# Kernel optimization log

Measured on AMD Instinct MI355X. Metric: run time of the kernel, lower is better.

## Reference

```python
import jax, jax.numpy as jnp
import numpy as np

B, LQ, LKV, LT, C, H = 4, 1024, 1344, 320, 768, 12
DH = C // H
SCALE = DH ** -0.5
HID = 4 * C
EPS = 1e-5


def _ln(x, g, b):
    m = jnp.mean(x, axis=-1, keepdims=True)
    v = jnp.mean((x - m) ** 2, axis=-1, keepdims=True)
    return (x - m) * jax.lax.rsqrt(v + EPS) * g + b


def setup_inputs() -> dict:
    key = jax.random.key(0)
    ks = jax.random.split(key, 16)
    s = lambda k, shape, sc=0.02: jax.random.normal(k, shape, dtype=jnp.float32) * sc
    return {
        "tem_mask": s(ks[0], (B, LT, C), 1.0),
        "q": s(ks[1], (B, LQ, C), 1.0),
        "kv": s(ks[2], (B, LKV, C), 1.0),
        "attn_pos": s(ks[3], (1, H, LQ, LKV), 1.0),
        "ln1q_g": jnp.ones((C,)), "ln1q_b": jnp.zeros((C,)),
        "ln1kv_g": jnp.ones((C,)), "ln1kv_b": jnp.zeros((C,)),
        "Wq": s(ks[4], (C, C)), "bq": jnp.zeros((C,)),
        "Wkv": s(ks[5], (C, 2 * C)), "bkv": jnp.zeros((2 * C,)),
        "Wp": s(ks[6], (C, C)), "bp": jnp.zeros((C,)),
        "ln2_g": jnp.ones((C,)), "ln2_b": jnp.zeros((C,)),
        "W1": s(ks[7], (C, HID)), "b1": jnp.zeros((HID,)),
        "W2": s(ks[8], (HID, C)), "b2": jnp.zeros((C,)),
    }


def reference(tem_mask, q, kv, attn_pos, ln1q_g, ln1q_b, ln1kv_g, ln1kv_b,
              Wq, bq, Wkv, bkv, Wp, bp, ln2_g, ln2_b, W1, b1, W2, b2):
    qn = _ln(q, ln1q_g, ln1q_b)
    kvn = _ln(kv, ln1kv_g, ln1kv_b)
    # projections (attn_pos_encoding_only branch)
    qh = (qn @ Wq + bq).reshape(B, LQ, H, DH).transpose(0, 2, 1, 3)  # (B,H,Lq,Dh)
    kvp = kvn @ Wkv + bkv
    k, v = kvp[:, :, :C], kvp[:, :, C:]
    v = v.at[:, :LT, :].add(tem_mask)  # add template mask to template tokens
    kh = k.reshape(B, LKV, H, DH).transpose(0, 2, 1, 3)
    vh = v.reshape(B, LKV, H, DH).transpose(0, 2, 1, 3)
    attn = jnp.einsum('bhqd,bhkd->bhqk', qh, kh) * SCALE + attn_pos
    attn = jax.nn.softmax(attn, axis=-1)
    x = jnp.einsum('bhqk,bhkd->bhqd', attn, vh)
    x = x.transpose(0, 2, 1, 3).reshape(B, LQ, C)
    x = x @ Wp + bp
    q = q + x  # residual 1 (drop_path = Identity, dropout eval)
    h = _ln(q, ln2_g, ln2_b)
    h = jax.nn.gelu(h @ W1 + b1, approximate=False)
    h = h @ W2 + b2
    return q + h
```

## Files before the change

### kernel.cpp

```cpp
#include <hip/hip_runtime.h>
#include <hip/hip_bf16.h>
#include <math.h>

typedef __bf16 bf16x8 __attribute__((ext_vector_type(8)));
typedef float f32x4 __attribute__((ext_vector_type(4)));

__device__ __forceinline__ __hip_bfloat16 f2bf(float v){ return __float2bfloat16(v); }

__device__ __forceinline__ void gload16(const void* g, void* l){
  __builtin_amdgcn_global_load_lds(
      (const __attribute__((address_space(1))) void*)g,
      (__attribute__((address_space(3))) void*)l, 16, 0, 0);
}

__global__ void transpose_f2b(const float* __restrict__ in,
                              __hip_bfloat16* __restrict__ out, int K, int N){
  __shared__ float tile[32][33];
  int tx = threadIdx.x, ty = threadIdx.y;
  int n0 = blockIdx.x*32, k0 = blockIdx.y*32;
#pragma unroll
  for(int i=0;i<4;i++) tile[ty+i*8][tx] = in[(size_t)(k0+ty+i*8)*N + n0+tx];
  __syncthreads();
#pragma unroll
  for(int i=0;i<4;i++) out[(size_t)(n0+ty+i*8)*K + k0+tx] = f2bf(tile[tx][ty+i*8]);
}

__global__ __launch_bounds__(256) void transpose_vt(const __hip_bfloat16* __restrict__ vbuf,
                                                    __hip_bfloat16* __restrict__ vt){
  __shared__ __hip_bfloat16 tl[64][72];
  const int bh = blockIdx.x;
  const int kt = blockIdx.y;
  const int b = bh / 12, h = bh % 12;
  const int tid = threadIdx.x;
  const int r = tid >> 3, c = (tid & 7) * 8;
#pragma unroll
  for(int j=0;j<2;j++){
    uint4 v = *(const uint4*)(vbuf + ((size_t)(b*1344 + kt*64 + r + j*32))*768 + h*64 + c);
    *(uint4*)&tl[r + j*32][c] = v;
  }
  __syncthreads();
#pragma unroll
  for(int j=0;j<2;j++){
    int d = r + j*32;
    __hip_bfloat16 tmp[8];
#pragma unroll
    for(int i=0;i<8;i++) tmp[i] = tl[c + i][d];
    *(uint4*)(vt + ((size_t)(bh*64 + d))*1344 + kt*64 + c) = *(const uint4*)tmp;
  }
}

__global__ __launch_bounds__(256) void ln_kernel(const float* __restrict__ in,
    const float* __restrict__ g, const float* __restrict__ b,
    __hip_bfloat16* __restrict__ out){
  int row = blockIdx.x, t = threadIdx.x;
  const float* rp = in + (size_t)row*768;
  float x0 = rp[t], x1 = rp[t+256], x2 = rp[t+512];
  float s = x0+x1+x2, ss = x0*x0+x1*x1+x2*x2;
#pragma unroll
  for(int o=32;o>0;o>>=1){ s += __shfl_down(s,o); ss += __shfl_down(ss,o); }
  __shared__ float red[10];
  if((t&63)==0){ red[t>>6]=s; red[4+(t>>6)]=ss; }
  __syncthreads();
  if(t==0){
    float S=red[0]+red[1]+red[2]+red[3], SS=red[4]+red[5]+red[6]+red[7];
    float m=S*(1.f/768.f);
    red[8]=m; red[9]=SS*(1.f/768.f)-m*m;
  }
  __syncthreads();
  float m=red[8], r=rsqrtf(red[9]+1e-5f);
  __hip_bfloat16* op = out + (size_t)row*768;
  op[t]     = f2bf((x0-m)*r*g[t]     + b[t]);
  op[t+256] = f2bf((x1-m)*r*g[t+256] + b[t+256]);
  op[t+512] = f2bf((x2-m)*r*g[t+512] + b[t+512]);
}

template<int BM, int EPI>
__global__ __launch_bounds__(256) void gemm_gl(
    const __hip_bfloat16* __restrict__ A, const __hip_bfloat16* __restrict__ BT,
    const float* __restrict__ bias, int M, int N, int K,
    void* __restrict__ out, const void* __restrict__ aux0, void* __restrict__ out2){
  constexpr int NF = (BM==128)?4:2;
  __shared__ char sA[2][BM*128];
  __shared__ char sB[2][128*128];
  const int tid = threadIdx.x;
  const int l = tid & 63, w = tid >> 6;
  const int lg = l >> 4, li = l & 15;
  const int wrow = (BM==128)? (w>>1)*64 : 0;
  const int wcol = (BM==128)? (w&1)*64 : w*32;
  const int bm = blockIdx.x * BM;
  const int bn = blockIdx.y * 128;
  const int arow = w*(BM/4) + (l>>3);
  const int brow = w*32 + (l>>3);
  const int scol = ((((l&7)*16) ^ ((l>>3)<<4)) >> 1);

  auto stage = [&](int buf, int kt){
    const int k0 = kt*64;
#pragma unroll
    for(int i=0;i<BM/32;i++)
      gload16(A  + (size_t)(bm+arow+i*8)*K + k0 + scol, sA[buf] + (w*(BM/4))*128 + i*1024);
#pragma unroll
    for(int i=0;i<4;i++)
      gload16(BT + (size_t)(bn+brow+i*8)*K + k0 + scol, sB[buf] + (w*32)*128 + i*1024);
  };

  f32x4 acc[4][NF] = {};
  const int nk = K >> 6;
  stage(0, 0);
  __syncthreads();
  for(int kt=0; kt<nk; ++kt){
    const int cur = kt & 1;
    if(kt+1 < nk) stage(cur^1, kt+1);
#pragma unroll
    for(int kk=0;kk<2;kk++){
      const int kb = kk*64 + lg*16;
      bf16x8 af[4], bfr[NF];
#pragma unroll
      for(int m=0;m<4;m++){
        int row = wrow+m*16+li;
        af[m] = *(const bf16x8*)(sA[cur] + row*128 + (kb ^ ((row&7)<<4)));
      }
#pragma unroll
      for(int n=0;n<NF;n++){
        int row = wcol+n*16+li;
        bfr[n] = *(const bf16x8*)(sB[cur] + row*128 + (kb ^ ((row&7)<<4)));
      }
#pragma unroll
      for(int m=0;m<4;m++)
#pragma unroll
        for(int n=0;n<NF;n++)
          acc[m][n] = __builtin_amdgcn_mfma_f32_16x16x32_bf16(af[m], bfr[n], acc[m][n],0,0,0);
    }
    __syncthreads();
  }
#pragma unroll
  for(int m=0;m<4;m++){
#pragma unroll
    for(int n=0;n<NF;n++){
#pragma unroll
      for(int r=0;r<4;r++){
        int row = bm + wrow + m*16 + lg*4 + r;
        int col = bn + wcol + n*16 + li;
        float v = acc[m][n][r] + bias[col];
        if constexpr(EPI==0){
          ((__hip_bfloat16*)out)[(size_t)row*N + col] = f2bf(v * 0.125f);
        } else if constexpr(EPI==1){
          if(col < 768){
            ((__hip_bfloat16*)out)[(size_t)row*768 + col] = f2bf(v);
          } else {
            int c = col - 768;
            int bb = row / 1344, ii = row % 1344;
            if(ii < 320) v += ((const float*)aux0)[((size_t)bb*320 + ii)*768 + c];
            ((__hip_bfloat16*)out2)[(size_t)row*768 + c] = f2bf(v);
          }
        } else if constexpr(EPI==2){
          v += ((const float*)aux0)[(size_t)row*N + col];
          ((float*)out)[(size_t)row*N + col] = v;
        } else if constexpr(EPI==3){
          float gl = 0.5f * v * (1.0f + erff(v * 0.70710678118654752f));
          ((__hip_bfloat16*)out)[(size_t)row*N + col] = f2bf(gl);
        } else {
          v += ((const float*)aux0)[(size_t)row*N + col];
          ((float*)out)[(size_t)row*N + col] = v;
        }
      }
    }
  }
}

__global__ __launch_bounds__(256) void attn_kernel(
    const __hip_bfloat16* __restrict__ qh,
    const __hip_bfloat16* __restrict__ kb,
    const __hip_bfloat16* __restrict__ vt,
    const float* __restrict__ pos,
    __hip_bfloat16* __restrict__ xo){
  __shared__ char sK[2][8192];
  __shared__ char sV[2][8192];
  __shared__ char sP[4][2048];
  const int bid = blockIdx.x;
  const int qt = bid & 15, h = (bid >> 4) % 12, b = bid / 192;
  const int q0 = qt * 64;
  const int tid = threadIdx.x;
  const int l = tid & 63, w = tid >> 6;
  const int lg = l >> 4, li = l & 15;

  const int srow = w*16 + (l>>3);
  const int soff = (((l&7)*16) ^ ((l>>3)<<4)) >> 1;
  const __hip_bfloat16* ksrc = kb + ((size_t)b*1344 + srow)*768 + h*64 + soff;
  const __hip_bfloat16* vsrc = vt + ((size_t)(b*12+h)*64 + srow)*1344 + soff;

  bf16x8 aq[2];
  {
    const char* qp = (const char*)(qh + ((size_t)(b*1024 + q0 + w*16 + li))*768 + h*64);
    aq[0] = *(const bf16x8*)(qp + lg*16);
    aq[1] = *(const bf16x8*)(qp + 64 + lg*16);
  }
  const size_t posbase = ((size_t)h*1024 + q0 + w*16 + lg*4)*1344 + li;

  f32x4 accO[4] = {};
  float mrun[4], lrun[4];
#pragma unroll
  for(int r=0;r<4;r++){ mrun[r] = -1e30f; lrun[r] = 0.f; }

  auto stage = [&](int buf, int t){
    const size_t ko = (size_t)t*64*768;
    const size_t vo = (size_t)t*64;
    gload16(ksrc + ko,          sK[buf] + w*2048);
    gload16(ksrc + ko + 8*768,  sK[buf] + w*2048 + 1024);
    gload16(vsrc + vo,          sV[buf] + w*2048);
    gload16(vsrc + vo + 8*1344, sV[buf] + w*2048 + 1024);
  };
  auto ldpos = [&](int t, float pr[4][4]){
    const float* pp = pos + posbase + (size_t)t*64;
#pragma unroll
    for(int n=0;n<4;n++)
#pragma unroll
      for(int r=0;r<4;r++)
        pr[n][r] = __builtin_nontemporal_load(pp + (size_t)r*1344 + n*16);
  };

  float posr[4][4];
  ldpos(0, posr);
  stage(0, 0);
  __syncthreads();

  char* sPw = sP[w];
  for(int t=0; t<21; ++t){
    const int cur = t & 1;
    f32x4 accS[4] = {};
#pragma unroll
    for(int kk=0; kk<2; ++kk){
      const int kbyte = kk*64 + lg*16;
#pragma unroll
      for(int n=0;n<4;n++){
        int row = n*16 + li;
        bf16x8 bkf = *(const bf16x8*)(sK[cur] + row*128 + (kbyte ^ ((row&7)<<4)));
        accS[n] = __builtin_amdgcn_mfma_f32_16x16x32_bf16(aq[kk], bkf, accS[n], 0,0,0);
      }
    }
    if(t < 20) stage(cur^1, t+1);
    float npos[4][4];
    if(t < 20) ldpos(t+1, npos);

    float p[4][4], mt[4];
#pragma unroll
    for(int r=0;r<4;r++) mt[r] = -1e30f;
#pragma unroll
    for(int n=0;n<4;n++)
#pragma unroll
      for(int r=0;r<4;r++){
        float s = accS[n][r] + posr[n][r];
        p[n][r] = s;
        mt[r] = fmaxf(mt[r], s);
      }
#pragma unroll
    for(int r=0;r<4;r++){
#pragma unroll
      for(int o=1;o<16;o<<=1) mt[r] = fmaxf(mt[r], __shfl_xor(mt[r], o));
      float mnew = fmaxf(mrun[r], mt[r]);
      float sf = __expf(mrun[r]-mnew);
      mrun[r] = mnew;
      lrun[r] *= sf;
#pragma unroll
      for(int n=0;n<4;n++) accO[n][r] *= sf;
      float rs = 0.f;
#pragma unroll
      for(int n=0;n<4;n++){ p[n][r] = __expf(p[n][r]-mnew); rs += p[n][r]; }
#pragma unroll
      for(int o=1;o<16;o<<=1) rs += __shfl_xor(rs, o);
      lrun[r] += rs;
    }
#pragma unroll
    for(int n=0;n<4;n++)
#pragma unroll
      for(int r=0;r<4;r++){
        int qi = lg*4 + r, kj = n*16 + li;
        *(__hip_bfloat16*)(sPw + qi*128 + ((kj*2) ^ ((qi&7)<<4))) = f2bf(p[n][r]);
      }
#pragma unroll
    for(int kk=0; kk<2; ++kk){
      const int kbyte = kk*64 + lg*16;
      bf16x8 pa = *(const bf16x8*)(sPw + li*128 + (kbyte ^ ((li&7)<<4)));
#pragma unroll
      for(int n=0;n<4;n++){
        int d = n*16 + li;
        bf16x8 bvf = *(const bf16x8*)(sV[cur] + d*128 + (kbyte ^ ((d&7)<<4)));
        accO[n] = __builtin_amdgcn_mfma_f32_16x16x32_bf16(pa, bvf, accO[n], 0,0,0);
      }
    }
    if(t < 20){
#pragma unroll
      for(int n=0;n<4;n++)
#pragma unroll
        for(int r=0;r<4;r++) posr[n][r] = npos[n][r];
    }
    __syncthreads();
  }
#pragma unroll
  for(int n=0;n<4;n++)
#pragma unroll
    for(int r=0;r<4;r++){
      int row = b*1024 + q0 + w*16 + lg*4 + r;
      int col = h*64 + n*16 + li;
      xo[(size_t)row*768 + col] = f2bf(accO[n][r] / lrun[r]);
    }
}

extern "C" void kernel_launch(void* const* d_in, const int* in_sizes, int n_in,
                              void* d_out, int out_size, void* d_ws, size_t ws_size,
                              hipStream_t stream){
  const float* tem   = (const float*)d_in[0];
  const float* qin   = (const float*)d_in[1];
  const float* kvin  = (const float*)d_in[2];
  const float* pos   = (const float*)d_in[3];
  const float* ln1qg = (const float*)d_in[4];
  const float* ln1qb = (const float*)d_in[5];
  const float* ln1kg = (const float*)d_in[6];
  const float* ln1kb = (const float*)d_in[7];
  const float* Wq    = (const float*)d_in[8];
  const float* bq    = (const float*)d_in[9];
  const float* Wkv   = (const float*)d_in[10];
  const float* bkv   = (const float*)d_in[11];
  const float* Wp    = (const float*)d_in[12];
  const float* bp    = (const float*)d_in[13];
  const float* ln2g  = (const float*)d_in[14];
  const float* ln2b  = (const float*)d_in[15];
  const float* W1    = (const float*)d_in[16];
  const float* b1    = (const float*)d_in[17];
  const float* W2    = (const float*)d_in[18];
  const float* b2    = (const float*)d_in[19];

  char* ws = (char*)d_ws; size_t off = 0;
  auto alloc = [&](size_t n){ char* p = ws + off; off = (off + n + 255) & ~(size_t)255; return p; };
  __hip_bfloat16* WqT  = (__hip_bfloat16*)alloc((size_t)768*768*2);
  __hip_bfloat16* WkvT = (__hip_bfloat16*)alloc((size_t)1536*768*2);
  __hip_bfloat16* WpT  = (__hip_bfloat16*)alloc((size_t)768*768*2);
  __hip_bfloat16* W1T  = (__hip_bfloat16*)alloc((size_t)3072*768*2);
  __hip_bfloat16* W2T  = (__hip_bfloat16*)alloc((size_t)768*3072*2);
  __hip_bfloat16* qn   = (__hip_bfloat16*)alloc((size_t)4096*768*2);
  char* poolBase = alloc((size_t)5376*768*2*3 + (size_t)4096*768*2);
  __hip_bfloat16* kvn  = (__hip_bfloat16*)poolBase;
  __hip_bfloat16* kbuf = kvn  + (size_t)5376*768;
  __hip_bfloat16* vbuf = kbuf + (size_t)5376*768;
  __hip_bfloat16* qhb  = vbuf + (size_t)5376*768;
  __hip_bfloat16* xat  = (__hip_bfloat16*)alloc((size_t)4096*768*2);
  float*          x1f  = (float*)alloc((size_t)4096*768*4);
  __hip_bfloat16* vt   = kvn;
  __hip_bfloat16* hln  = qn;
  __hip_bfloat16* h1   = kvn;

  dim3 tb(32,8);
  transpose_f2b<<<dim3(768/32, 768/32),  tb, 0, stream>>>(Wq,  WqT,  768, 768);
  transpose_f2b<<<dim3(1536/32, 768/32), tb, 0, stream>>>(Wkv, WkvT, 768, 1536);
  transpose_f2b<<<dim3(768/32, 768/32),  tb, 0, stream>>>(Wp,  WpT,  768, 768);
  transpose_f2b<<<dim3(3072/32, 768/32), tb, 0, stream>>>(W1,  W1T,  768, 3072);
  transpose_f2b<<<dim3(768/32, 3072/32), tb, 0, stream>>>(W2,  W2T,  3072, 768);

  ln_kernel<<<4096, 256, 0, stream>>>(qin,  ln1qg, ln1qb, qn);
  ln_kernel<<<5376, 256, 0, stream>>>(kvin, ln1kg, ln1kb, kvn);

  gemm_gl<64,0> <<<dim3(64, 6),  256, 0, stream>>>(qn,  WqT,  bq,  4096, 768,  768,  qhb, nullptr, nullptr);
  gemm_gl<128,1><<<dim3(42, 12), 256, 0, stream>>>(kvn, WkvT, bkv, 5376, 1536, 768,  kbuf, tem, vbuf);
  transpose_vt<<<dim3(48, 21), 256, 0, stream>>>(vbuf, vt);

  attn_kernel<<<768, 256, 0, stream>>>(qhb, kbuf, vt, pos, xat);

  gemm_gl<64,2> <<<dim3(64, 6),  256, 0, stream>>>(xat, WpT,  bp,  4096, 768,  768,  x1f, qin, nullptr);
  ln_kernel<<<4096, 256, 0, stream>>>(x1f, ln2g, ln2b, hln);
  gemm_gl<128,3><<<dim3(32, 24), 256, 0, stream>>>(hln, W1T,  b1,  4096, 3072, 768,  h1, nullptr, nullptr);
  gemm_gl<64,4> <<<dim3(64, 6),  256, 0, stream>>>(h1,  W2T,  b2,  4096, 768,  3072, (float*)d_out, x1f, nullptr);
}
```

Before: 258.3 us.

## Restructure attention blocks to share attn_pos tile across batches with 32-key steps

The attention kernel now uses 512-thread blocks covering one head and a 32-row query tile for all four batch elements. Each wave pair handles one batch, and the grid mapping is arranged so that blocks sharing the same attn_pos rows are adjacent. The key tile shrinks from 64 to 32, giving 42 iterations unrolled in pairs with ping-pong position registers. The loop issues prefetches before compute and replaces __syncthreads with an explicit vmcnt wait plus a raw barrier. The aim is better pos reuse through cache and finer-grained overlap, at the cost of more iterations and barriers, a tricky manual waitcnt, and half the block count.

```diff
diff --git a/kernel.cpp b/kernel.cpp
--- a/kernel.cpp
+++ b/kernel.cpp
@@ -167,34 +167,38 @@
   }
 }
 
-__global__ __launch_bounds__(256) void attn_kernel(
+__global__ __launch_bounds__(512) void attn_kernel(
     const __hip_bfloat16* __restrict__ qh,
     const __hip_bfloat16* __restrict__ kb,
     const __hip_bfloat16* __restrict__ vt,
     const float* __restrict__ pos,
     __hip_bfloat16* __restrict__ xo){
-  __shared__ char sK[2][8192];
-  __shared__ char sV[2][8192];
-  __shared__ char sP[4][2048];
+  __shared__ char sK[2][4][4096];
+  __shared__ char sV[2][4][4096];
+  __shared__ char sP[8][1024];
   const int bid = blockIdx.x;
-  const int qt = bid & 15, h = (bid >> 4) % 12, b = bid / 192;
-  const int q0 = qt * 64;
+  const int u = (bid & 7)*3 + ((bid >> 3) >> 4);
+  const int v = (bid >> 3) & 15;
+  const int h = u >> 1;
+  const int q0 = ((u & 1)*16 + v) * 32;
   const int tid = threadIdx.x;
   const int l = tid & 63, w = tid >> 6;
+  const int bt = w >> 1, qhv = w & 1;
   const int lg = l >> 4, li = l & 15;
 
-  const int srow = w*16 + (l>>3);
-  const int soff = (((l&7)*16) ^ ((l>>3)<<4)) >> 1;
-  const __hip_bfloat16* ksrc = kb + ((size_t)b*1344 + srow)*768 + h*64 + soff;
-  const __hip_bfloat16* vsrc = vt + ((size_t)(b*12+h)*64 + srow)*1344 + soff;
+  const int kelem = ((((l&7)*16) ^ ((l>>3)<<4)) >> 1);
+  const int velem = ((((l&3)*16) ^ (((l>>2)&3)<<4)) >> 1);
+  const __hip_bfloat16* ksrc = kb + ((size_t)bt*1344 + qhv*16 + (l>>3))*768 + h*64 + kelem;
+  const __hip_bfloat16* vsrc = vt + (((size_t)(bt*12+h))*64 + qhv*32 + (l>>2))*1344 + velem;
+  char* sKb = nullptr; char* sVb = nullptr;
 
   bf16x8 aq[2];
   {
-    const char* qp = (const char*)(qh + ((size_t)(b*1024 + q0 + w*16 + li))*768 + h*64);
+    const char* qp = (const char*)(qh + ((size_t)(bt*1024 + q0 + qhv*16 + li))*768 + h*64);
     aq[0] = *(const bf16x8*)(qp + lg*16);
     aq[1] = *(const bf16x8*)(qp + 64 + lg*16);
   }
-  const size_t posbase = ((size_t)h*1024 + q0 + w*16 + lg*4)*1344 + li;
+  const size_t posbase = ((size_t)h*1024 + q0 + qhv*16 + lg*4)*1344 + li;
 
   f32x4 accO[4] = {};
   float mrun[4], lrun[4];
@@ -202,50 +206,52 @@
   for(int r=0;r<4;r++){ mrun[r] = -1e30f; lrun[r] = 0.f; }
 
   auto stage = [&](int buf, int t){
-    const size_t ko = (size_t)t*64*768;
-    const size_t vo = (size_t)t*64;
-    gload16(ksrc + ko,          sK[buf] + w*2048);
-    gload16(ksrc + ko + 8*768,  sK[buf] + w*2048 + 1024);
-    gload16(vsrc + vo,          sV[buf] + w*2048);
-    gload16(vsrc + vo + 8*1344, sV[buf] + w*2048 + 1024);
+    const size_t ko = (size_t)t*32*768;
+    const size_t vo = (size_t)t*32;
+#pragma unroll
+    for(int i=0;i<2;i++)
+      gload16(ksrc + ko + (size_t)i*8*768, sK[buf][bt] + qhv*2048 + i*1024);
+#pragma unroll
+    for(int i=0;i<2;i++)
+      gload16(vsrc + vo + (size_t)i*16*1344, sV[buf][bt] + qhv*2048 + i*1024);
   };
-  auto ldpos = [&](int t, float pr[4][4]){
-    const float* pp = pos + posbase + (size_t)t*64;
-#pragma unroll
-    for(int n=0;n<4;n++)
+  auto ldpos = [&](int t, float pr[2][4]){
+    const float* pp = pos + posbase + (size_t)t*32;
+#pragma unroll
+    for(int n=0;n<2;n++)
 #pragma unroll
       for(int r=0;r<4;r++)
         pr[n][r] = __builtin_nontemporal_load(pp + (size_t)r*1344 + n*16);
   };
 
-  float posr[4][4];
-  ldpos(0, posr);
+  char* sPw = sP[w];
+  float pA[2][4], pB[2][4];
+  ldpos(0, pA);
   stage(0, 0);
   __syncthreads();
 
-  char* sPw = sP[w];
-  for(int t=0; t<21; ++t){
-    const int cur = t & 1;
-    f32x4 accS[4] = {};
+  auto body = [&](int t, int cur, float posr[2][4], float npos[2][4]){
+    const bool more = (t < 41);
+    if(more) stage(cur^1, t+1);
+    asm volatile("" ::: "memory");
+    if(more) ldpos(t+1, npos);
+
+    f32x4 accS[2] = {};
 #pragma unroll
     for(int kk=0; kk<2; ++kk){
       const int kbyte = kk*64 + lg*16;
 #pragma unroll
-      for(int n=0;n<4;n++){
+      for(int n=0;n<2;n++){
         int row = n*16 + li;
-        bf16x8 bkf = *(const bf16x8*)(sK[cur] + row*128 + (kbyte ^ ((row&7)<<4)));
+        bf16x8 bkf = *(const bf16x8*)(sK[cur][bt] + row*128 + (kbyte ^ ((row&7)<<4)));
         accS[n] = __builtin_amdgcn_mfma_f32_16x16x32_bf16(aq[kk], bkf, accS[n], 0,0,0);
       }
     }
-    if(t < 20) stage(cur^1, t+1);
-    float npos[4][4];
-    if(t < 20) ldpos(t+1, npos);
-
-    float p[4][4], mt[4];
+    float p[2][4], mt[4];
 #pragma unroll
     for(int r=0;r<4;r++) mt[r] = -1e30f;
 #pragma unroll
-    for(int n=0;n<4;n++)
+    for(int n=0;n<2;n++)
 #pragma unroll
       for(int r=0;r<4;r++){
         float s = accS[n][r] + posr[n][r];
@@ -264,42 +270,39 @@
       for(int n=0;n<4;n++) accO[n][r] *= sf;
       float rs = 0.f;
 #pragma unroll
-      for(int n=0;n<4;n++){ p[n][r] = __expf(p[n][r]-mnew); rs += p[n][r]; }
+      for(int n=0;n<2;n++){ p[n][r] = __expf(p[n][r]-mnew); rs += p[n][r]; }
 #pragma unroll
       for(int o=1;o<16;o<<=1) rs += __shfl_xor(rs, o);
       lrun[r] += rs;
     }
 #pragma unroll
-    for(int n=0;n<4;n++)
+    for(int n=0;n<2;n++)
 #pragma unroll
       for(int r=0;r<4;r++){
         int qi = lg*4 + r, kj = n*16 + li;
-        *(__hip_bfloat16*)(sPw + qi*128 + ((kj*2) ^ ((qi&7)<<4))) = f2bf(p[n][r]);
-      }
-#pragma unroll
-    for(int kk=0; kk<2; ++kk){
-      const int kbyte = kk*64 + lg*16;
-      bf16x8 pa = *(const bf16x8*)(sPw + li*128 + (kbyte ^ ((li&7)<<4)));
-#pragma unroll
-      for(int n=0;n<4;n++){
-        int d = n*16 + li;
-        bf16x8 bvf = *(const bf16x8*)(sV[cur] + d*128 + (kbyte ^ ((d&7)<<4)));
-        accO[n] = __builtin_amdgcn_mfma_f32_16x16x32_bf16(pa, bvf, accO[n], 0,0,0);
-      }
-    }
-    if(t < 20){
-#pragma unroll
-      for(int n=0;n<4;n++)
-#pragma unroll
-        for(int r=0;r<4;r++) posr[n][r] = npos[n][r];
-    }
-    __syncthreads();
-  }
+        *(__hip_bfloat16*)(sPw + qi*64 + ((kj*2) ^ (r<<4))) = f2bf(p[n][r]);
+      }
+    bf16x8 pa = *(const bf16x8*)(sPw + li*64 + ((lg*16) ^ ((li&3)<<4)));
+#pragma unroll
+    for(int n=0;n<4;n++){
+      int d = n*16 + li;
+      bf16x8 bvf = *(const bf16x8*)(sV[cur][bt] + d*64 + ((lg*16) ^ ((d&3)<<4)));
+      accO[n] = __builtin_amdgcn_mfma_f32_16x16x32_bf16(pa, bvf, accO[n], 0,0,0);
+    }
+    if(more) asm volatile("s_waitcnt vmcnt(8)" ::: "memory");
+    __builtin_amdgcn_s_barrier();
+  };
+
+  for(int tt=0; tt<21; ++tt){
+    body(2*tt,   0, pA, pB);
+    body(2*tt+1, 1, pB, pA);
+  }
+
 #pragma unroll
   for(int n=0;n<4;n++)
 #pragma unroll
     for(int r=0;r<4;r++){
-      int row = b*1024 + q0 + w*16 + lg*4 + r;
+      int row = bt*1024 + q0 + qhv*16 + lg*4 + r;
       int col = h*64 + n*16 + li;
       xo[(size_t)row*768 + col] = f2bf(accO[n][r] / lrun[r]);
     }
@@ -362,7 +365,7 @@
   gemm_gl<128,1><<<dim3(42, 12), 256, 0, stream>>>(kvn, WkvT, bkv, 5376, 1536, 768,  kbuf, tem, vbuf);
   transpose_vt<<<dim3(48, 21), 256, 0, stream>>>(vbuf, vt);
 
-  attn_kernel<<<768, 256, 0, stream>>>(qhb, kbuf, vt, pos, xat);
+  attn_kernel<<<384, 512, 0, stream>>>(qhb, kbuf, vt, pos, xat);
 
   gemm_gl<64,2> <<<dim3(64, 6),  256, 0, stream>>>(xat, WpT,  bp,  4096, 768,  768,  x1f, qin, nullptr);
   ln_kernel<<<4096, 256, 0, stream>>>(x1f, ln2g, ln2b, hln);
```

New measurement: 299.6 us. +16.0%, slower.

## Merge weight transposes and LayerNorms into single launches; use 64x64 GEMM tiles

Applied to the files above, without the earlier changes.

The five weight-transpose launches become one kernel that picks its matrix from the block index. The two input LayerNorm launches become one kernel covering q and kv rows. The GEMM template gains a BN parameter, and the three N=768 GEMMs move to 64x64 tiles with a 2x2 warp layout, doubling the grid to 768 blocks. This is meant to cut launch overhead and raise occupancy across the CUs on the narrow GEMMs, at the cost of less reuse per tile.

```diff
diff --git a/kernel.cpp b/kernel.cpp
--- a/kernel.cpp
+++ b/kernel.cpp
@@ -13,11 +13,23 @@
       (__attribute__((address_space(3))) void*)l, 16, 0, 0);
 }
 
-__global__ void transpose_f2b(const float* __restrict__ in,
-                              __hip_bfloat16* __restrict__ out, int K, int N){
+__global__ void transpose_all(const float* __restrict__ Wq, const float* __restrict__ Wkv,
+                              const float* __restrict__ Wp, const float* __restrict__ W1,
+                              const float* __restrict__ W2,
+                              __hip_bfloat16* __restrict__ oq, __hip_bfloat16* __restrict__ okv,
+                              __hip_bfloat16* __restrict__ op_, __hip_bfloat16* __restrict__ o1,
+                              __hip_bfloat16* __restrict__ o2){
   __shared__ float tile[32][33];
+  const int bid = blockIdx.x;
+  const float* in; __hip_bfloat16* out; int K, N, local;
+  if(bid < 576)        { in=Wq;  out=oq;  K=768;  N=768;  local=bid; }
+  else if(bid < 1728)  { in=Wkv; out=okv; K=768;  N=1536; local=bid-576; }
+  else if(bid < 2304)  { in=Wp;  out=op_; K=768;  N=768;  local=bid-1728; }
+  else if(bid < 4608)  { in=W1;  out=o1;  K=768;  N=3072; local=bid-2304; }
+  else                 { in=W2;  out=o2;  K=3072; N=768;  local=bid-4608; }
+  const int nbx = N/32;
+  const int n0 = (local % nbx)*32, k0 = (local / nbx)*32;
   int tx = threadIdx.x, ty = threadIdx.y;
-  int n0 = blockIdx.x*32, k0 = blockIdx.y*32;
 #pragma unroll
   for(int i=0;i<4;i++) tile[ty+i*8][tx] = in[(size_t)(k0+ty+i*8)*N + n0+tx];
   __syncthreads();
@@ -49,48 +61,63 @@
   }
 }
 
+__device__ __forceinline__ void ln_body(const float* rp, const float* g, const float* b,
+                                        __hip_bfloat16* op, int t){
+  float x0 = rp[t], x1 = rp[t+256], x2 = rp[t+512];
+  float s = x0+x1+x2, ss = x0*x0+x1*x1+x2*x2;
+#pragma unroll
+  for(int o=32;o>0;o>>=1){ s += __shfl_down(s,o); ss += __shfl_down(ss,o); }
+  __shared__ float red[10];
+  if((t&63)==0){ red[t>>6]=s; red[4+(t>>6)]=ss; }
+  __syncthreads();
+  if(t==0){
+    float S=red[0]+red[1]+red[2]+red[3], SS=red[4]+red[5]+red[6]+red[7];
+    float m=S*(1.f/768.f);
+    red[8]=m; red[9]=SS*(1.f/768.f)-m*m;
+  }
+  __syncthreads();
+  float m=red[8], r=rsqrtf(red[9]+1e-5f);
+  op[t]     = f2bf((x0-m)*r*g[t]     + b[t]);
+  op[t+256] = f2bf((x1-m)*r*g[t+256] + b[t+256]);
+  op[t+512] = f2bf((x2-m)*r*g[t+512] + b[t+512]);
+}
+
+__global__ __launch_bounds__(256) void ln_qkv(const float* __restrict__ q, const float* __restrict__ kv,
+    const float* __restrict__ qg, const float* __restrict__ qb,
+    const float* __restrict__ kg, const float* __restrict__ kb2,
+    __hip_bfloat16* __restrict__ qn, __hip_bfloat16* __restrict__ kvn){
+  int row = blockIdx.x, t = threadIdx.x;
+  if(row < 4096) ln_body(q + (size_t)row*768, qg, qb, qn + (size_t)row*768, t);
+  else { row -= 4096; ln_body(kv + (size_t)row*768, kg, kb2, kvn + (size_t)row*768, t); }
+}
+
 __global__ __launch_bounds__(256) void ln_kernel(const float* __restrict__ in,
     const float* __restrict__ g, const float* __restrict__ b,
     __hip_bfloat16* __restrict__ out){
   int row = blockIdx.x, t = threadIdx.x;
-  const float* rp = in + (size_t)row*768;
-  float x0 = rp[t], x1 = rp[t+256], x2 = rp[t+512];
-  float s = x0+x1+x2, ss = x0*x0+x1*x1+x2*x2;
-#pragma unroll
-  for(int o=32;o>0;o>>=1){ s += __shfl_down(s,o); ss += __shfl_down(ss,o); }
-  __shared__ float red[10];
-  if((t&63)==0){ red[t>>6]=s; red[4+(t>>6)]=ss; }
-  __syncthreads();
-  if(t==0){
-    float S=red[0]+red[1]+red[2]+red[3], SS=red[4]+red[5]+red[6]+red[7];
-    float m=S*(1.f/768.f);
-    red[8]=m; red[9]=SS*(1.f/768.f)-m*m;
-  }
-  __syncthreads();
-  float m=red[8], r=rsqrtf(red[9]+1e-5f);
-  __hip_bfloat16* op = out + (size_t)row*768;
-  op[t]     = f2bf((x0-m)*r*g[t]     + b[t]);
-  op[t+256] = f2bf((x1-m)*r*g[t+256] + b[t+256]);
-  op[t+512] = f2bf((x2-m)*r*g[t+512] + b[t+512]);
-}
-
-template<int BM, int EPI>
+  ln_body(in + (size_t)row*768, g, b, out + (size_t)row*768, t);
+}
+
+template<int BM, int BN, int EPI>
 __global__ __launch_bounds__(256) void gemm_gl(
     const __hip_bfloat16* __restrict__ A, const __hip_bfloat16* __restrict__ BT,
     const float* __restrict__ bias, int M, int N, int K,
     void* __restrict__ out, const void* __restrict__ aux0, void* __restrict__ out2){
-  constexpr int NF = (BM==128)?4:2;
+  constexpr int WR = (BM==128 || BN==64) ? 2 : 1;
+  constexpr int WC = 4/WR;
+  constexpr int MF = BM/(WR*16);
+  constexpr int NF = BN/(WC*16);
   __shared__ char sA[2][BM*128];
-  __shared__ char sB[2][128*128];
+  __shared__ char sB[2][BN*128];
   const int tid = threadIdx.x;
   const int l = tid & 63, w = tid >> 6;
   const int lg = l >> 4, li = l & 15;
-  const int wrow = (BM==128)? (w>>1)*64 : 0;
-  const int wcol = (BM==128)? (w&1)*64 : w*32;
+  const int wrow = (WR==2) ? (w>>1)*(BM/2) : 0;
+  const int wcol = (WC==2) ? (w&1)*(BN/2) : w*(BN/4);
   const int bm = blockIdx.x * BM;
-  const int bn = blockIdx.y * 128;
+  const int bn = blockIdx.y * BN;
   const int arow = w*(BM/4) + (l>>3);
-  const int brow = w*32 + (l>>3);
+  const int brow = w*(BN/4) + (l>>3);
   const int scol = ((((l&7)*16) ^ ((l>>3)<<4)) >> 1);
 
   auto stage = [&](int buf, int kt){
@@ -99,11 +126,11 @@
     for(int i=0;i<BM/32;i++)
       gload16(A  + (size_t)(bm+arow+i*8)*K + k0 + scol, sA[buf] + (w*(BM/4))*128 + i*1024);
 #pragma unroll
-    for(int i=0;i<4;i++)
-      gload16(BT + (size_t)(bn+brow+i*8)*K + k0 + scol, sB[buf] + (w*32)*128 + i*1024);
+    for(int i=0;i<BN/32;i++)
+      gload16(BT + (size_t)(bn+brow+i*8)*K + k0 + scol, sB[buf] + (w*(BN/4))*128 + i*1024);
   };
 
-  f32x4 acc[4][NF] = {};
+  f32x4 acc[MF][NF] = {};
   const int nk = K >> 6;
   stage(0, 0);
   __syncthreads();
@@ -113,9 +140,9 @@
 #pragma unroll
     for(int kk=0;kk<2;kk++){
       const int kb = kk*64 + lg*16;
-      bf16x8 af[4], bfr[NF];
-#pragma unroll
-      for(int m=0;m<4;m++){
+      bf16x8 af[MF], bfr[NF];
+#pragma unroll
+      for(int m=0;m<MF;m++){
         int row = wrow+m*16+li;
         af[m] = *(const bf16x8*)(sA[cur] + row*128 + (kb ^ ((row&7)<<4)));
       }
@@ -125,7 +152,7 @@
         bfr[n] = *(const bf16x8*)(sB[cur] + row*128 + (kb ^ ((row&7)<<4)));
       }
 #pragma unroll
-      for(int m=0;m<4;m++)
+      for(int m=0;m<MF;m++)
 #pragma unroll
         for(int n=0;n<NF;n++)
           acc[m][n] = __builtin_amdgcn_mfma_f32_16x16x32_bf16(af[m], bfr[n], acc[m][n],0,0,0);
@@ -133,7 +160,7 @@
     __syncthreads();
   }
 #pragma unroll
-  for(int m=0;m<4;m++){
+  for(int m=0;m<MF;m++){
 #pragma unroll
     for(int n=0;n<NF;n++){
 #pragma unroll
@@ -348,24 +375,17 @@
   __hip_bfloat16* hln  = qn;
   __hip_bfloat16* h1   = kvn;
 
-  dim3 tb(32,8);
-  transpose_f2b<<<dim3(768/32, 768/32),  tb, 0, stream>>>(Wq,  WqT,  768, 768);
-  transpose_f2b<<<dim3(1536/32, 768/32), tb, 0, stream>>>(Wkv, WkvT, 768, 1536);
-  transpose_f2b<<<dim3(768/32, 768/32),  tb, 0, stream>>>(Wp,  WpT,  768, 768);
-  transpose_f2b<<<dim3(3072/32, 768/32), tb, 0, stream>>>(W1,  W1T,  768, 3072);
-  transpose_f2b<<<dim3(768/32, 3072/32), tb, 0, stream>>>(W2,  W2T,  3072, 768);
-
-  ln_kernel<<<4096, 256, 0, stream>>>(qin,  ln1qg, ln1qb, qn);
-  ln_kernel<<<5376, 256, 0, stream>>>(kvin, ln1kg, ln1kb, kvn);
-
-  gemm_gl<64,0> <<<dim3(64, 6),  256, 0, stream>>>(qn,  WqT,  bq,  4096, 768,  768,  qhb, nullptr, nullptr);
-  gemm_gl<128,1><<<dim3(42, 12), 256, 0, stream>>>(kvn, WkvT, bkv, 5376, 1536, 768,  kbuf, tem, vbuf);
+  transpose_all<<<6912, dim3(32,8), 0, stream>>>(Wq, Wkv, Wp, W1, W2, WqT, WkvT, WpT, W1T, W2T);
+  ln_qkv<<<4096+5376, 256, 0, stream>>>(qin, kvin, ln1qg, ln1qb, ln1kg, ln1kb, qn, kvn);
+
+  gemm_gl<64,64,0>  <<<dim3(64, 12), 256, 0, stream>>>(qn,  WqT,  bq,  4096, 768,  768,  qhb, nullptr, nullptr);
+  gemm_gl<128,128,1><<<dim3(42, 12), 256, 0, stream>>>(kvn, WkvT, bkv, 5376, 1536, 768,  kbuf, tem, vbuf);
   transpose_vt<<<dim3(48, 21), 256, 0, stream>>>(vbuf, vt);
 
   attn_kernel<<<768, 256, 0, stream>>>(qhb, kbuf, vt, pos, xat);
 
-  gemm_gl<64,2> <<<dim3(64, 6),  256, 0, stream>>>(xat, WpT,  bp,  4096, 768,  768,  x1f, qin, nullptr);
+  gemm_gl<64,64,2>  <<<dim3(64, 12), 256, 0, stream>>>(xat, WpT,  bp,  4096, 768,  768,  x1f, qin, nullptr);
   ln_kernel<<<4096, 256, 0, stream>>>(x1f, ln2g, ln2b, hln);
-  gemm_gl<128,3><<<dim3(32, 24), 256, 0, stream>>>(hln, W1T,  b1,  4096, 3072, 768,  h1, nullptr, nullptr);
-  gemm_gl<64,4> <<<dim3(64, 6),  256, 0, stream>>>(h1,  W2T,  b2,  4096, 768,  3072, (float*)d_out, x1f, nullptr);
-}
+  gemm_gl<128,128,3><<<dim3(32, 24), 256, 0, stream>>>(hln, W1T,  b1,  4096, 3072, 768,  h1, nullptr, nullptr);
+  gemm_gl<64,64,4>  <<<dim3(64, 12), 256, 0, stream>>>(h1,  W2T,  b2,  4096, 768,  3072, (float*)d_out, x1f, nullptr);
+}
```

After: 248.9 us. 3.6% less time.
